# Kernel tuning notes

Measured on AMD Instinct MI355X. Metric: run time of the kernel, lower is better.

The kernel has to match this reference:

```python
import jax, jax.numpy as jnp
import numpy as np

N = 102400   # total nodes (256 graphs x 400 nodes)
E = 1600000  # total edges
B = 256      # number of graphs
F_IN = 4
H = 128
GH = 120     # GRU hidden
C_IN = 84
L = 100


def setup_inputs() -> dict:
    key = jax.random.key(0)
    ks = jax.random.split(key, 32)
    rn = lambda k, shape, sc: (jax.random.normal(k, shape, jnp.float32) * sc)
    s = lambda fan: 1.0 / np.sqrt(fan)
    inp = {}
    inp["x"] = rn(ks[0], (N, F_IN), 1.0)
    inp["edge_index"] = jax.random.randint(ks[1], (2, E), 0, N)
    inp["batch"] = jnp.repeat(jnp.arange(B), N // B)  # sorted segment ids, no empty segments
    inp["target01"] = rn(ks[2], (B, C_IN, L), 1.0)
    # GraphConv params: out = segsum(x_j) @ W_rel + b + x @ W_root
    inp["W1_rel"] = rn(ks[3], (F_IN, H), s(F_IN)); inp["W1_root"] = rn(ks[4], (F_IN, H), s(F_IN)); inp["b1"] = jnp.zeros((H,), jnp.float32)
    inp["W2_rel"] = rn(ks[5], (H, H), s(H)); inp["W2_root"] = rn(ks[6], (H, H), s(H)); inp["b2"] = jnp.zeros((H,), jnp.float32)
    inp["W3_rel"] = rn(ks[7], (H, H), s(H)); inp["W3_root"] = rn(ks[8], (H, H), s(H)); inp["b3"] = jnp.zeros((H,), jnp.float32)
    # Conv1d(84 -> 128, k=3)
    inp["Wc"] = rn(ks[9], (H, C_IN, 3), s(C_IN * 3)); inp["bc"] = jnp.zeros((H,), jnp.float32)
    # Bidirectional GRU(128 -> 120)
    inp["Wih_f"] = rn(ks[10], (3 * GH, H), s(H)); inp["Whh_f"] = rn(ks[11], (3 * GH, GH), s(GH))
    inp["bih_f"] = jnp.zeros((3 * GH,), jnp.float32); inp["bhh_f"] = jnp.zeros((3 * GH,), jnp.float32)
    inp["Wih_b"] = rn(ks[12], (3 * GH, H), s(H)); inp["Whh_b"] = rn(ks[13], (3 * GH, GH), s(GH))
    inp["bih_b"] = jnp.zeros((3 * GH,), jnp.float32); inp["bhh_b"] = jnp.zeros((3 * GH,), jnp.float32)
    # Dense head
    inp["Wd1"] = rn(ks[14], (4816, 102), s(4816)); inp["bd1"] = jnp.zeros((102,), jnp.float32)
    inp["Wd3"] = rn(ks[15], (102, 2), s(102)); inp["bd3"] = jnp.zeros((2,), jnp.float32)
    return inp


def _graph_conv(x, src, dst, W_rel, b, W_root, n):
    # PyG GraphConv, aggr='add': lin_rel(sum_j x_j) + lin_root(x)
    agg = jax.ops.segment_sum(x[src], dst, num_segments=n)
    return agg @ W_rel + b + x @ W_root


def _gru_dir(xs, Wih, Whh, bih, bhh, reverse):
    # xs: [T, B, D] -> [T, B, GH]; PyTorch GRU cell equations
    h0 = jnp.zeros((xs.shape[1], Whh.shape[1]), xs.dtype)
    def step(h, xt):
        gi = xt @ Wih.T + bih
        gh = h @ Whh.T + bhh
        ir, iz, i_n = jnp.split(gi, 3, axis=-1)
        hr, hz, h_n = jnp.split(gh, 3, axis=-1)
        r = jax.nn.sigmoid(ir + hr)
        z = jax.nn.sigmoid(iz + hz)
        n = jnp.tanh(i_n + r * h_n)
        h2 = (1.0 - z) * n + z * h
        return h2, h2
    _, ys = jax.lax.scan(step, h0, xs, reverse=reverse)
    return ys


def reference(x, edge_index, batch, target01, W1_rel, W1_root, b1, W2_rel, W2_root, b2,
              W3_rel, W3_root, b3, Wc, bc, Wih_f, Whh_f, bih_f, bhh_f,
              Wih_b, Whh_b, bih_b, bhh_b, Wd1, bd1, Wd3, bd3):
    src, dst = edge_index[0], edge_index[1]
    n = x.shape[0]
    x1 = jax.nn.relu(_graph_conv(x, src, dst, W1_rel, b1, W1_root, n))
    x2 = jax.nn.relu(_graph_conv(x1, src, dst, W2_rel, b2, W2_root, n))
    x3 = jax.nn.relu(_graph_conv(x2, src, dst, W3_rel, b3, W3_root, n)) + x1  # residual
    x4 = jax.nn.relu(_graph_conv(x3, src, dst, W3_rel, b3, W3_root, n))      # conv3 reused
    gmax = jax.ops.segment_max(x4, batch, num_segments=B)
    gsum = jax.ops.segment_sum(x4, batch, num_segments=B)
    cnt = jax.ops.segment_sum(jnp.ones((n, 1), x4.dtype), batch, num_segments=B)
    g = jnp.concatenate([gmax, gsum / cnt], axis=1)  # [B, 256]
    # Conv1d (valid, k=3) + relu
    xl = jax.lax.conv_general_dilated(target01, Wc, (1,), 'VALID',
                                      dimension_numbers=('NCH', 'OIH', 'NCH')) + bc[None, :, None]
    xl = jax.nn.relu(xl)  # [B, 128, 98]
    Lp = (xl.shape[2] // 5) * 5
    xt = xl[:, :, :Lp].reshape(B, H, Lp // 5, 5).mean(-1)  # avg_pool1d k=5 -> [B,128,19]
    xs = jnp.transpose(xt, (2, 0, 1))  # [T, B, 128]
    yf = _gru_dir(xs, Wih_f, Whh_f, bih_f, bhh_f, False)
    yb = _gru_dir(xs, Wih_b, Whh_b, bih_b, bhh_b, True)
    y = jnp.concatenate([yf, yb], axis=-1)            # [T, B, 240]
    y = jnp.transpose(y, (1, 0, 2)).reshape(B, -1)    # [B, 4560]
    xc = jnp.concatenate([g, y], axis=1)              # [B, 4816]
    xc = jax.nn.relu(xc @ Wd1 + bd1)
    return jax.nn.log_softmax(xc @ Wd3 + bd3, axis=-1)
```

## Files before the change

kernel.cpp:

```cpp
#include <hip/hip_runtime.h>
#include <cmath>

constexpr int N_NODES = 102400;
constexpr int N_EDGES = 1600000;
constexpr int BGR     = 256;
constexpr int NPG     = 400;
constexpr int F_IN    = 4;
constexpr int H       = 128;
constexpr int GH      = 120;
constexpr int G3      = 360;
constexpr int C_IN    = 84;
constexpr int LSEQ    = 100;
constexpr int TT      = 19;
constexpr int DHEAD   = 4816;
constexpr int D1O     = 102;
constexpr int KCOMB   = 256;
constexpr int CAP     = 64;
constexpr int NXCD    = 8;
constexpr int NPX     = N_NODES / NXCD;
constexpr int SGRP    = 104;

using short8 = __attribute__((ext_vector_type(8))) short;
using f32x4  = __attribute__((ext_vector_type(4))) float;

__device__ __forceinline__ short f2bf(float f) {
    unsigned u = __float_as_uint(f);
    u += 0x7FFFu + ((u >> 16) & 1u);
    return (short)(u >> 16);
}
__device__ __forceinline__ float bf2f(short s) {
    return __uint_as_float(((unsigned)(unsigned short)s) << 16);
}

__device__ __forceinline__ void tr_seg(const float* __restrict__ in, float* __restrict__ out,
                                       int R, int C, int i) {
    if (i < R * C) {
        int r = i / C, c = i % C;
        out[(long)c * R + r] = in[i];
    }
}
__device__ __forceinline__ void wbt_seg(const float* __restrict__ Wrel, const float* __restrict__ Wroot,
                                        short* __restrict__ WBT, int i) {
    if (i < H * KCOMB) {
        int h = i >> 8, k = i & 255;
        float v = (k < H) ? Wrel[k * H + h] : Wroot[(k - H) * H + h];
        WBT[h * KCOMB + k] = f2bf(v);
    }
}
constexpr int PB0 = 126;
constexpr int PB1 = 180;
constexpr int PB2 = 180;
constexpr int PB3 = 169;
constexpr int PB4 = 169;
constexpr int PB6 = 128;
constexpr int PB7 = 128;
constexpr int PREP_BLOCKS = PB0+PB1+PB2+PB3+PB4+PB6+PB7;

__global__ void prep_fused(const float* Wc, float* WCT,
                           const float* Wihf, float* WIHTF,
                           const float* Wihb, float* WIHTB,
                           const float* Whhf, float* WHHTF,
                           const float* Whhb, float* WHHTB,
                           const float* W2rel, const float* W2root, short* WBT2,
                           const float* W3rel, const float* W3root, short* WBT3) {
    int b = blockIdx.x;
    int t = threadIdx.x;
    if (b < PB0) { tr_seg(Wc,   WCT,   128, 252, b * 256 + t); return; }  b -= PB0;
    if (b < PB1) { tr_seg(Wihf, WIHTF, G3,  H,   b * 256 + t); return; }  b -= PB1;
    if (b < PB2) { tr_seg(Wihb, WIHTB, G3,  H,   b * 256 + t); return; }  b -= PB2;
    if (b < PB3) { tr_seg(Whhf, WHHTF, G3,  GH,  b * 256 + t); return; }  b -= PB3;
    if (b < PB4) { tr_seg(Whhb, WHHTB, G3,  GH,  b * 256 + t); return; }  b -= PB4;
    if (b < PB6) { wbt_seg(W2rel, W2root, WBT2, b * 256 + t); return; }   b -= PB6;
    wbt_seg(W3rel, W3root, WBT3, b * 256 + t);
}

__global__ __launch_bounds__(256) void transpose_tiled(const float* __restrict__ in,
                                                       float* __restrict__ out, int R, int C) {
    __shared__ float tile[32][33];
    const int rb = blockIdx.x * 32, cb = blockIdx.y * 32;
    const int tx = threadIdx.x & 31, ty = threadIdx.x >> 5;
#pragma unroll
    for (int yy = 0; yy < 32; yy += 8) {
        int r = rb + ty + yy, c = cb + tx;
        if (r < R && c < C) tile[ty + yy][tx] = in[(long)r * C + c];
    }
    __syncthreads();
#pragma unroll
    for (int yy = 0; yy < 32; yy += 8) {
        int ro = cb + ty + yy, co = rb + tx;
        if (ro < C && co < R) out[(long)ro * R + co] = tile[tx][ty + yy];
    }
}

__global__ __launch_bounds__(256) void xcd_scatter(const int* __restrict__ src,
                                                   const int* __restrict__ dst,
                                                   int* __restrict__ cnt,
                                                   int* __restrict__ csr, int E) {
    const int g   = blockIdx.x & (NXCD - 1);
    const int grp = blockIdx.x >> 3;
    const int nlo = g * NPX, nhi = nlo + NPX;
    const int stride = SGRP * 256 * 4;
    for (int e = (grp * 256 + threadIdx.x) * 4; e + 3 < E; e += stride) {
        const int4 s = *(const int4*)(src + e);
        const int4 d = *(const int4*)(dst + e);
        if (d.x >= nlo && d.x < nhi) { int p = atomicAdd(&cnt[d.x], 1); csr[((long)d.x << 6) + p] = s.x; }
        if (d.y >= nlo && d.y < nhi) { int p = atomicAdd(&cnt[d.y], 1); csr[((long)d.y << 6) + p] = s.y; }
        if (d.z >= nlo && d.z < nhi) { int p = atomicAdd(&cnt[d.z], 1); csr[((long)d.z << 6) + p] = s.z; }
        if (d.w >= nlo && d.w < nhi) { int p = atomicAdd(&cnt[d.w], 1); csr[((long)d.w << 6) + p] = s.w; }
    }
}

__global__ __launch_bounds__(256) void agg4_csr(const int* __restrict__ cnt,
                                                const int* __restrict__ csr,
                                                const float* __restrict__ x,
                                                float* __restrict__ agg) {
    int i = blockIdx.x * 256 + threadIdx.x;
    int n = i >> 2, c = i & 3;
    const int cn = cnt[n];
    const int* idx = csr + ((long)n << 6);
    float acc = 0.f;
    for (int j = 0; j < cn; ++j) acc += x[(long)idx[j] * 4 + c];
    agg[i] = acc;
}

__global__ void gc1_transform(const float* __restrict__ agg4, const float* __restrict__ x,
                              const float* __restrict__ Wrel, const float* __restrict__ Wroot,
                              const float* __restrict__ bias, float* __restrict__ out,
                              short* __restrict__ outb) {
    long i = (long)blockIdx.x * 256 + threadIdx.x;
    int h = (int)(i & (H - 1));
    long n = i >> 7;
    const float4 a  = *(const float4*)(agg4 + n * 4);
    const float4 xv = *(const float4*)(x    + n * 4);
    float acc = bias[h]
        + a.x  * Wrel[0 * H + h] + a.y  * Wrel[1 * H + h]
        + a.z  * Wrel[2 * H + h] + a.w  * Wrel[3 * H + h]
        + xv.x * Wroot[0 * H + h] + xv.y * Wroot[1 * H + h]
        + xv.z * Wroot[2 * H + h] + xv.w * Wroot[3 * H + h];
    float v = fmaxf(acc, 0.f);
    out[i] = v;
    outb[i] = f2bf(v);
}

__global__ __launch_bounds__(256) void agg128_bf(const int* __restrict__ cnt,
                                                 const int* __restrict__ csr,
                                                 const short* __restrict__ xb,
                                                 short* __restrict__ aggb) {
    const int lane = threadIdx.x & 15;
    const int n = blockIdx.x * 16 + (threadIdx.x >> 4);
    const int cn = cnt[n];
    const int* idx = csr + ((long)n << 6);
    float acc[8];
#pragma unroll
    for (int q = 0; q < 8; ++q) acc[q] = 0.f;
    int j = 0;
    for (; j + 3 < cn; j += 4) {
        const int4 ii = *(const int4*)(idx + j);
        const short8 r0 = *(const short8*)(xb + (long)ii.x * H + lane * 8);
        const short8 r1 = *(const short8*)(xb + (long)ii.y * H + lane * 8);
        const short8 r2 = *(const short8*)(xb + (long)ii.z * H + lane * 8);
        const short8 r3 = *(const short8*)(xb + (long)ii.w * H + lane * 8);
#pragma unroll
        for (int q = 0; q < 8; ++q)
            acc[q] += (bf2f(r0[q]) + bf2f(r1[q])) + (bf2f(r2[q]) + bf2f(r3[q]));
    }
    for (; j < cn; ++j) {
        const short8 r0 = *(const short8*)(xb + (long)idx[j] * H + lane * 8);
#pragma unroll
        for (int q = 0; q < 8; ++q) acc[q] += bf2f(r0[q]);
    }
    short8 o;
#pragma unroll
    for (int q = 0; q < 8; ++q) o[q] = f2bf(acc[q]);
    *(short8*)(aggb + (long)n * H + lane * 8) = o;
}

template <int RES, int OUTF, int OUTB>
__global__ __launch_bounds__(256) void gc_mfma(
        const short* __restrict__ aggb, const short* __restrict__ xinb,
        const short* __restrict__ WBT, const float* __restrict__ bias,
        const float* __restrict__ res, float* __restrict__ outf,
        short* __restrict__ outb) {
    const int wid   = threadIdx.x >> 6;
    const int lane  = threadIdx.x & 63;
    const int l15   = lane & 15;
    const int kslot = lane >> 4;
    const long n0   = (long)blockIdx.x * 128 + wid * 32;

    f32x4 acc[2][8];
#pragma unroll
    for (int i = 0; i < 2; ++i)
#pragma unroll
        for (int j = 0; j < 8; ++j) acc[i][j] = (f32x4){0.f, 0.f, 0.f, 0.f};

#pragma unroll
    for (int ks = 0; ks < 8; ++ks) {
        const short* srcb = (ks < 4) ? aggb : xinb;
        const int koff = (ks < 4 ? ks * 32 : (ks - 4) * 32) + kslot * 8;
        short8 afr[2];
#pragma unroll
        for (int rt = 0; rt < 2; ++rt)
            afr[rt] = *(const short8*)(srcb + (n0 + rt * 16 + l15) * H + koff);
        const int kb = ks * 32 + kslot * 8;
        short8 bfr[8];
#pragma unroll
        for (int ct = 0; ct < 8; ++ct)
            bfr[ct] = *(const short8*)(WBT + (long)(ct * 16 + l15) * KCOMB + kb);
#pragma unroll
        for (int rt = 0; rt < 2; ++rt)
#pragma unroll
            for (int ct = 0; ct < 8; ++ct)
                acc[rt][ct] = __builtin_amdgcn_mfma_f32_16x16x32_bf16(
                    afr[rt], bfr[ct], acc[rt][ct], 0, 0, 0);
    }

#pragma unroll
    for (int rt = 0; rt < 2; ++rt) {
        const long rbase = n0 + rt * 16 + kslot * 4;
#pragma unroll
        for (int ct = 0; ct < 8; ++ct) {
            const int h = ct * 16 + l15;
            const float bv = bias[h];
#pragma unroll
            for (int r = 0; r < 4; ++r) {
                const long rowi = rbase + r;
                float v = fmaxf(acc[rt][ct][r] + bv, 0.f);
                if (RES) v += res[rowi * H + h];
                if (OUTF) outf[rowi * H + h] = v;
                if (OUTB) outb[rowi * H + h] = f2bf(v);
            }
        }
    }
}

__global__ __launch_bounds__(512) void pool_kernel(const float* __restrict__ x4, float* __restrict__ xc) {
    int g = blockIdx.x;
    int h = threadIdx.x & 127;
    int part = threadIdx.x >> 7;
    const float* base = x4 + ((long)g * NPG + part * 100) * H + h;
    float mx = -INFINITY, sm = 0.f;
#pragma unroll 4
    for (int i = 0; i < 100; ++i) {
        float v = base[(long)i * H];
        mx = fmaxf(mx, v);
        sm += v;
    }
    __shared__ float smx[4][128], ssm[4][128];
    smx[part][h] = mx; ssm[part][h] = sm;
    __syncthreads();
    if (part == 0) {
        float m = fmaxf(fmaxf(smx[0][h], smx[1][h]), fmaxf(smx[2][h], smx[3][h]));
        float s = ssm[0][h] + ssm[1][h] + ssm[2][h] + ssm[3][h];
        xc[(long)g * DHEAD + h] = m;
        xc[(long)g * DHEAD + H + h] = s * (1.f / NPG);
    }
}

__global__ __launch_bounds__(128) void conv1d_pool(const float* __restrict__ in,
                                                   const float* __restrict__ WcT,
                                                   const float* __restrict__ bc,
                                                   float* __restrict__ xs) {
    int p = blockIdx.x;
    int b = blockIdx.y;
    int o = threadIdx.x;
    __shared__ float sIn[C_IN][8];
    const float* ib = in + (long)b * C_IN * LSEQ;
    for (int idx = threadIdx.x; idx < C_IN * 7; idx += 128) {
        int c = idx / 7, j = idx % 7;
        sIn[c][j] = ib[c * LSEQ + 5 * p + j];
    }
    __syncthreads();
    float a0 = 0, a1 = 0, a2 = 0, a3 = 0, a4 = 0;
    for (int c = 0; c < C_IN; ++c) {
        float i0 = sIn[c][0], i1 = sIn[c][1], i2 = sIn[c][2], i3 = sIn[c][3];
        float i4 = sIn[c][4], i5 = sIn[c][5], i6 = sIn[c][6];
        float w0 = WcT[(c * 3 + 0) * H + o];
        float w1 = WcT[(c * 3 + 1) * H + o];
        float w2 = WcT[(c * 3 + 2) * H + o];
        a0 += w0 * i0 + w1 * i1 + w2 * i2;
        a1 += w0 * i1 + w1 * i2 + w2 * i3;
        a2 += w0 * i2 + w1 * i3 + w2 * i4;
        a3 += w0 * i3 + w1 * i4 + w2 * i5;
        a4 += w0 * i4 + w1 * i5 + w2 * i6;
    }
    float bcv = bc[o];
    float r = fmaxf(a0 + bcv, 0.f) + fmaxf(a1 + bcv, 0.f) + fmaxf(a2 + bcv, 0.f)
            + fmaxf(a3 + bcv, 0.f) + fmaxf(a4 + bcv, 0.f);
    xs[((long)p * BGR + b) * H + o] = r * 0.2f;
}

__global__ __launch_bounds__(384) void gi_gemm(const float* __restrict__ xs,
                                               const float* __restrict__ WihT,
                                               const float* __restrict__ bih,
                                               float* __restrict__ gi) {
    const long r0 = (long)blockIdx.x * 16;
    const int g = threadIdx.x;
    __shared__ __align__(16) float sX[16][H];
    for (int idx = threadIdx.x; idx < 16 * H; idx += 384)
        sX[idx >> 7][idx & (H - 1)] = xs[r0 * H + idx];
    __syncthreads();
    if (g >= G3) return;
    const float bv = bih[g];
    float acc[16];
#pragma unroll
    for (int r = 0; r < 16; ++r) acc[r] = bv;
    for (int k = 0; k < H; k += 4) {
        float w0 = WihT[(k + 0) * G3 + g], w1 = WihT[(k + 1) * G3 + g];
        float w2 = WihT[(k + 2) * G3 + g], w3 = WihT[(k + 3) * G3 + g];
#pragma unroll
        for (int r = 0; r < 16; ++r) {
            float4 xv = *(const float4*)&sX[r][k];
            acc[r] += xv.x * w0 + xv.y * w1 + xv.z * w2 + xv.w * w3;
        }
    }
#pragma unroll
    for (int r = 0; r < 16; ++r)
        gi[(r0 + r) * G3 + g] = acc[r];
}

__device__ __forceinline__ float sigmoidf_(float x) { return 1.f / (1.f + expf(-x)); }

__global__ __launch_bounds__(384) void gru_kernel(
        const float* __restrict__ giF, const float* __restrict__ giB,
        const float* __restrict__ WhhTF, const float* __restrict__ WhhTB,
        const float* __restrict__ bhhF, const float* __restrict__ bhhB,
        float* __restrict__ xc) {
    const int b = blockIdx.x & (BGR - 1);
    const int dir = blockIdx.x >> 8;
    const float* gi   = dir ? giB : giF;
    const float* WhhT = dir ? WhhTB : WhhTF;
    const float* bhh  = dir ? bhhB : bhhF;
    const int g = threadIdx.x;
    const int gc = g < G3 ? g : (G3 - 1);

    float w[GH];
#pragma unroll
    for (int k = 0; k < GH; ++k) w[k] = WhhT[(long)k * G3 + gc];
    const float bh = bhh[gc];

    __shared__ __align__(16) float sh[GH];
    __shared__ float sgh[G3];
    if (g < GH) sh[g] = 0.f;
    __syncthreads();

    for (int tt = 0; tt < TT; ++tt) {
        const int t = dir ? (TT - 1 - tt) : tt;
        float acc = bh;
#pragma unroll
        for (int k4 = 0; k4 < GH / 4; ++k4) {
            float4 hv = *(const float4*)&sh[k4 * 4];
            acc += hv.x * w[k4 * 4] + hv.y * w[k4 * 4 + 1]
                 + hv.z * w[k4 * 4 + 2] + hv.w * w[k4 * 4 + 3];
        }
        if (g < G3) sgh[g] = acc;
        __syncthreads();
        if (g < GH) {
            const float* gib = gi + ((long)t * BGR + b) * G3;
            float r = sigmoidf_(gib[g] + sgh[g]);
            float z = sigmoidf_(gib[GH + g] + sgh[GH + g]);
            float n = tanhf(gib[2 * GH + g] + r * sgh[2 * GH + g]);
            float h2 = (1.f - z) * n + z * sh[g];
            sh[g] = h2;
            xc[(long)b * DHEAD + 256 + t * 240 + dir * GH + g] = h2;
        }
        __syncthreads();
    }
}

__global__ __launch_bounds__(256) void dense1(const float* __restrict__ xc,
                                              const float* __restrict__ Wd1T,
                                              const float* __restrict__ bd1,
                                              float* __restrict__ d1) {
    const int wid  = blockIdx.x * 4 + (threadIdx.x >> 6);
    const int lane = threadIdx.x & 63;
    const int jg = wid % 26;
    const int bg = wid / 26;
    const int j0 = jg * 4, b0 = bg * 8;

    float acc[4][8];
#pragma unroll
    for (int jj = 0; jj < 4; ++jj)
#pragma unroll
        for (int bb = 0; bb < 8; ++bb) acc[jj][bb] = 0.f;

    for (int i = lane; i < DHEAD / 4; i += 64) {
        float4 wv[4], xv[8];
#pragma unroll
        for (int jj = 0; jj < 4; ++jj) {
            int j = j0 + jj; if (j > D1O - 1) j = D1O - 1;
            wv[jj] = *(const float4*)(Wd1T + (long)j * DHEAD + i * 4);
        }
#pragma unroll
        for (int bb = 0; bb < 8; ++bb)
            xv[bb] = *(const float4*)(xc + (long)(b0 + bb) * DHEAD + i * 4);
#pragma unroll
        for (int jj = 0; jj < 4; ++jj)
#pragma unroll
            for (int bb = 0; bb < 8; ++bb)
                acc[jj][bb] += wv[jj].x * xv[bb].x + wv[jj].y * xv[bb].y
                             + wv[jj].z * xv[bb].z + wv[jj].w * xv[bb].w;
    }
#pragma unroll
    for (int m = 32; m >= 1; m >>= 1)
#pragma unroll
        for (int jj = 0; jj < 4; ++jj)
#pragma unroll
            for (int bb = 0; bb < 8; ++bb)
                acc[jj][bb] += __shfl_xor(acc[jj][bb], m, 64);
    if (lane < 32) {
        const int jj = lane >> 3, bb = lane & 7;
        const int j = j0 + jj;
        if (j < D1O)
            d1[(long)(b0 + bb) * D1O + j] = fmaxf(acc[jj][bb] + bd1[j], 0.f);
    }
}

__global__ void final_head(const float* __restrict__ d1, const float* __restrict__ Wd3,
                           const float* __restrict__ bd3, float* __restrict__ out) {
    int b = threadIdx.x;
    if (b >= BGR) return;
    float v0 = bd3[0], v1 = bd3[1];
    for (int k = 0; k < D1O; ++k) {
        float xv = d1[(long)b * D1O + k];
        v0 += xv * Wd3[k * 2 + 0];
        v1 += xv * Wd3[k * 2 + 1];
    }
    float m = fmaxf(v0, v1);
    float lse = m + logf(expf(v0 - m) + expf(v1 - m));
    out[b * 2 + 0] = v0 - lse;
    out[b * 2 + 1] = v1 - lse;
}

extern "C" void kernel_launch(void* const* d_in, const int* in_sizes, int n_in,
                              void* d_out, int out_size, void* d_ws, size_t ws_size,
                              hipStream_t stream) {
    const float* x      = (const float*)d_in[0];
    const int*   ei     = (const int*)d_in[1];
    const float* tgt    = (const float*)d_in[3];
    const float* W1rel  = (const float*)d_in[4];
    const float* W1root = (const float*)d_in[5];
    const float* b1     = (const float*)d_in[6];
    const float* W2rel  = (const float*)d_in[7];
    const float* W2root = (const float*)d_in[8];
    const float* b2     = (const float*)d_in[9];
    const float* W3rel  = (const float*)d_in[10];
    const float* W3root = (const float*)d_in[11];
    const float* b3     = (const float*)d_in[12];
    const float* Wc     = (const float*)d_in[13];
    const float* bc     = (const float*)d_in[14];
    const float* Wih_f  = (const float*)d_in[15];
    const float* Whh_f  = (const float*)d_in[16];
    const float* bih_f  = (const float*)d_in[17];
    const float* bhh_f  = (const float*)d_in[18];
    const float* Wih_b  = (const float*)d_in[19];
    const float* Whh_b  = (const float*)d_in[20];
    const float* bih_b  = (const float*)d_in[21];
    const float* bhh_b  = (const float*)d_in[22];
    const float* Wd1    = (const float*)d_in[23];
    const float* bd1    = (const float*)d_in[24];
    const float* Wd3    = (const float*)d_in[25];
    const float* bd3    = (const float*)d_in[26];

    const int* srcI = ei;
    const int* dstI = ei + N_EDGES;

    float* ws = (float*)d_ws;
    size_t off = 0;
    float* AGG4  = ws + off; off += (size_t)N_NODES * 4;
    float* X1    = ws + off; off += (size_t)N_NODES * H;
    float* XS    = ws + off; off += (size_t)TT * BGR * H;
    float* GIF   = ws + off; off += (size_t)TT * BGR * G3;
    float* GIB   = ws + off; off += (size_t)TT * BGR * G3;
    float* XC    = ws + off; off += (size_t)BGR * DHEAD;
    float* D1    = ws + off; off += (size_t)BGR * D1O + 2;
    float* WCT   = ws + off; off += (size_t)C_IN * 3 * H;
    float* WIHTF = ws + off; off += (size_t)H * G3;
    float* WIHTB = ws + off; off += (size_t)H * G3;
    float* WHHTF = ws + off; off += (size_t)GH * G3;
    float* WHHTB = ws + off; off += (size_t)GH * G3;
    float* WD1T  = ws + off; off += (size_t)DHEAD * D1O;
    off = (off + 3) & ~(size_t)3;
    short* WBT2  = (short*)(ws + off); off += (size_t)H * KCOMB / 2;
    short* WBT3  = (short*)(ws + off); off += (size_t)H * KCOMB / 2;
    short* AGGB  = (short*)(ws + off); off += (size_t)N_NODES * H / 2;
    short* X1B   = (short*)(ws + off); off += (size_t)N_NODES * H / 2;
    short* X2B   = (short*)(ws + off); off += (size_t)N_NODES * H / 2;
    short* X3B   = (short*)(ws + off); off += (size_t)N_NODES * H / 2;
    int* ibase   = (int*)(ws + off);
    int* CNT     = ibase;
    int* CSR     = ibase + N_NODES;

    prep_fused<<<PREP_BLOCKS, 256, 0, stream>>>(Wc, WCT, Wih_f, WIHTF, Wih_b, WIHTB,
                                                Whh_f, WHHTF, Whh_b, WHHTB,
                                                W2rel, W2root, WBT2, W3rel, W3root, WBT3);
    transpose_tiled<<<dim3((DHEAD + 31) / 32, (D1O + 31) / 32), 256, 0, stream>>>(Wd1, WD1T, DHEAD, D1O);

    hipMemsetAsync(CNT, 0, (size_t)N_NODES * sizeof(int), stream);
    xcd_scatter<<<NXCD * SGRP, 256, 0, stream>>>(srcI, dstI, CNT, CSR, N_EDGES);

    agg4_csr<<<(N_NODES * 4) / 256, 256, 0, stream>>>(CNT, CSR, x, AGG4);
    gc1_transform<<<(N_NODES * H) / 256, 256, 0, stream>>>(AGG4, x, W1rel, W1root, b1, X1, X1B);

    agg128_bf<<<N_NODES / 16, 256, 0, stream>>>(CNT, CSR, X1B, AGGB);
    gc_mfma<0, 0, 1><<<N_NODES / 128, 256, 0, stream>>>(AGGB, X1B, WBT2, b2, nullptr, nullptr, X2B);

    agg128_bf<<<N_NODES / 16, 256, 0, stream>>>(CNT, CSR, X2B, AGGB);
    gc_mfma<1, 0, 1><<<N_NODES / 128, 256, 0, stream>>>(AGGB, X2B, WBT3, b3, X1, nullptr, X3B);

    agg128_bf<<<N_NODES / 16, 256, 0, stream>>>(CNT, CSR, X3B, AGGB);
    gc_mfma<0, 1, 0><<<N_NODES / 128, 256, 0, stream>>>(AGGB, X3B, WBT3, b3, nullptr, X1, nullptr);

    pool_kernel<<<BGR, 512, 0, stream>>>(X1, XC);

    conv1d_pool<<<dim3(TT, BGR), 128, 0, stream>>>(tgt, WCT, bc, XS);

    gi_gemm<<<(TT * BGR) / 16, 384, 0, stream>>>(XS, WIHTF, bih_f, GIF);
    gi_gemm<<<(TT * BGR) / 16, 384, 0, stream>>>(XS, WIHTB, bih_b, GIB);

    gru_kernel<<<2 * BGR, 384, 0, stream>>>(GIF, GIB, WHHTF, WHHTB, bhh_f, bhh_b, XC);

    dense1<<<(26 * 32) / 4, 256, 0, stream>>>(XC, WD1T, bd1, D1);
    final_head<<<1, 256, 0, stream>>>(D1, Wd3, bd3, (float*)d_out);
}
```

Measured before the change: 714.3 us.

## Store bf16 node features in column-group slices for cache-local gathers

Bf16 node-feature and aggregate buffers move from row-major [N,128] to eight column-group slices of [N,16]. The aggregation kernel now launches one block per column group and node tile, so each gather pass touches only a 3.2 MB slice that can stay resident in L2/MALL, at the cost of 32-byte random reads instead of 256-byte rows. Producers in gc1_transform and gc_mfma and the MFMA A-operand loads are rewritten to match the sliced layout, and CSR indices are now re-read once per column group.

```diff
diff --git a/kernel.cpp b/kernel.cpp
--- a/kernel.cpp
+++ b/kernel.cpp
@@ -19,6 +19,8 @@
 constexpr int NXCD    = 8;
 constexpr int NPX     = N_NODES / NXCD;
 constexpr int SGRP    = 104;
+constexpr int NCG     = 8;
+constexpr long SLICE  = (long)N_NODES * 16;
 
 using short8 = __attribute__((ext_vector_type(8))) short;
 using f32x4  = __attribute__((ext_vector_type(4))) float;
@@ -139,40 +141,43 @@
         + xv.z * Wroot[2 * H + h] + xv.w * Wroot[3 * H + h];
     float v = fmaxf(acc, 0.f);
     out[i] = v;
-    outb[i] = f2bf(v);
-}
-
-__global__ __launch_bounds__(256) void agg128_bf(const int* __restrict__ cnt,
+    outb[(long)(h >> 4) * SLICE + n * 16 + (h & 15)] = f2bf(v);
+}
+
+__global__ __launch_bounds__(256) void agg128_cg(const int* __restrict__ cnt,
                                                  const int* __restrict__ csr,
                                                  const short* __restrict__ xb,
                                                  short* __restrict__ aggb) {
-    const int lane = threadIdx.x & 15;
-    const int n = blockIdx.x * 16 + (threadIdx.x >> 4);
+    const int cg = blockIdx.x & (NCG - 1);
+    const int nb = blockIdx.x >> 3;
+    const int n  = nb * 128 + (threadIdx.x >> 1);
+    const int lane = threadIdx.x & 1;
     const int cn = cnt[n];
     const int* idx = csr + ((long)n << 6);
+    const short* xs = xb + (long)cg * SLICE + lane * 8;
     float acc[8];
 #pragma unroll
     for (int q = 0; q < 8; ++q) acc[q] = 0.f;
     int j = 0;
     for (; j + 3 < cn; j += 4) {
         const int4 ii = *(const int4*)(idx + j);
-        const short8 r0 = *(const short8*)(xb + (long)ii.x * H + lane * 8);
-        const short8 r1 = *(const short8*)(xb + (long)ii.y * H + lane * 8);
-        const short8 r2 = *(const short8*)(xb + (long)ii.z * H + lane * 8);
-        const short8 r3 = *(const short8*)(xb + (long)ii.w * H + lane * 8);
+        const short8 r0 = *(const short8*)(xs + (long)ii.x * 16);
+        const short8 r1 = *(const short8*)(xs + (long)ii.y * 16);
+        const short8 r2 = *(const short8*)(xs + (long)ii.z * 16);
+        const short8 r3 = *(const short8*)(xs + (long)ii.w * 16);
 #pragma unroll
         for (int q = 0; q < 8; ++q)
             acc[q] += (bf2f(r0[q]) + bf2f(r1[q])) + (bf2f(r2[q]) + bf2f(r3[q]));
     }
     for (; j < cn; ++j) {
-        const short8 r0 = *(const short8*)(xb + (long)idx[j] * H + lane * 8);
+        const short8 r0 = *(const short8*)(xs + (long)idx[j] * 16);
 #pragma unroll
         for (int q = 0; q < 8; ++q) acc[q] += bf2f(r0[q]);
     }
     short8 o;
 #pragma unroll
     for (int q = 0; q < 8; ++q) o[q] = f2bf(acc[q]);
-    *(short8*)(aggb + (long)n * H + lane * 8) = o;
+    *(short8*)(aggb + (long)cg * SLICE + (long)n * 16 + lane * 8) = o;
 }
 
 template <int RES, int OUTF, int OUTB>
@@ -197,10 +202,11 @@
     for (int ks = 0; ks < 8; ++ks) {
         const short* srcb = (ks < 4) ? aggb : xinb;
         const int koff = (ks < 4 ? ks * 32 : (ks - 4) * 32) + kslot * 8;
+        const short* sbase = srcb + (long)(koff >> 4) * SLICE + (koff & 15);
         short8 afr[2];
 #pragma unroll
         for (int rt = 0; rt < 2; ++rt)
-            afr[rt] = *(const short8*)(srcb + (n0 + rt * 16 + l15) * H + koff);
+            afr[rt] = *(const short8*)(sbase + (n0 + rt * 16 + l15) * 16);
         const int kb = ks * 32 + kslot * 8;
         short8 bfr[8];
 #pragma unroll
@@ -227,7 +233,7 @@
                 float v = fmaxf(acc[rt][ct][r] + bv, 0.f);
                 if (RES) v += res[rowi * H + h];
                 if (OUTF) outf[rowi * H + h] = v;
-                if (OUTB) outb[rowi * H + h] = f2bf(v);
+                if (OUTB) outb[(long)ct * SLICE + rowi * 16 + l15] = f2bf(v);
             }
         }
     }
@@ -501,13 +507,13 @@
     agg4_csr<<<(N_NODES * 4) / 256, 256, 0, stream>>>(CNT, CSR, x, AGG4);
     gc1_transform<<<(N_NODES * H) / 256, 256, 0, stream>>>(AGG4, x, W1rel, W1root, b1, X1, X1B);
 
-    agg128_bf<<<N_NODES / 16, 256, 0, stream>>>(CNT, CSR, X1B, AGGB);
+    agg128_cg<<<NCG * (N_NODES / 128), 256, 0, stream>>>(CNT, CSR, X1B, AGGB);
     gc_mfma<0, 0, 1><<<N_NODES / 128, 256, 0, stream>>>(AGGB, X1B, WBT2, b2, nullptr, nullptr, X2B);
 
-    agg128_bf<<<N_NODES / 16, 256, 0, stream>>>(CNT, CSR, X2B, AGGB);
+    agg128_cg<<<NCG * (N_NODES / 128), 256, 0, stream>>>(CNT, CSR, X2B, AGGB);
     gc_mfma<1, 0, 1><<<N_NODES / 128, 256, 0, stream>>>(AGGB, X2B, WBT3, b3, X1, nullptr, X3B);
 
-    agg128_bf<<<N_NODES / 16, 256, 0, stream>>>(CNT, CSR, X3B, AGGB);
+    agg128_cg<<<NCG * (N_NODES / 128), 256, 0, stream>>>(CNT, CSR, X3B, AGGB);
     gc_mfma<0, 1, 0><<<N_NODES / 128, 256, 0, stream>>>(AGGB, X3B, WBT3, b3, nullptr, X1, nullptr);
 
     pool_kernel<<<BGR, 512, 0, stream>>>(X1, XC);
```

Result: slower. 819.1 us (+14.7%).
